# Kernel optimization log

Measured on AMD Instinct MI355X. Metric: run time of the kernel, lower is better.

## Reference

```python
import jax, jax.numpy as jnp
import numpy as np
import math

D, H, DK, DFF, B, T, K = 512, 8, 64, 2048, 8, 512, 31
P = 2 * T - 1  # rel-pos length


def _ln(x, g, b, eps=1e-5):
    mu = jnp.mean(x, -1, keepdims=True)
    var = jnp.var(x, -1, keepdims=True)
    return (x - mu) * jax.lax.rsqrt(var + eps) * g + b


def _silu(x):
    return x * jax.nn.sigmoid(x)


def _rel_shift(x):
    # x: [B,H,T,P] -> NeMo-style relative shift
    b, h, t, p = x.shape
    x = jnp.pad(x, ((0, 0), (0, 0), (0, 0), (1, 0)))
    x = x.reshape(b, h, p + 1, t)
    return x[:, :, 1:, :].reshape(b, h, t, p)


def _forward(x, pos_emb, ln1_g, ln1_b, ff1_w1, ff1_b1, ff1_w2, ff1_b2,
             lna_g, lna_b, wq, bq, wk, bk, wv, bv, wo, bo, wpos, pbu, pbv,
             lnc_g, lnc_b, pw1_w, pw1_b, dw_w, dw_b, cln_g, cln_b, pw2_w, pw2_b,
             ln2_g, ln2_b, ff2_w1, ff2_b1, ff2_w2, ff2_b2, lno_g, lno_b):
    b, t, d = x.shape
    h, dk = pbu.shape
    # FF1 (half-step residual)
    r = x
    y = _ln(x, ln1_g, ln1_b)
    y = _silu(y @ ff1_w1 + ff1_b1) @ ff1_w2 + ff1_b2
    r = r + 0.5 * y
    # Rel-pos multi-head attention
    y = _ln(r, lna_g, lna_b)
    q = (y @ wq + bq).reshape(b, t, h, dk)
    k = (y @ wk + bk).reshape(b, t, h, dk)
    v = (y @ wv + bv).reshape(b, t, h, dk)
    p = (pos_emb @ wpos).reshape(pos_emb.shape[0], -1, h, dk)[0]  # [P,H,dk]
    ac = jnp.einsum('bthd,bshd->bhts', q + pbu, k)
    bd = jnp.einsum('bthd,phd->bhtp', q + pbv, p)
    bd = _rel_shift(bd)[..., :t]
    attn = jax.nn.softmax((ac + bd) / math.sqrt(dk), axis=-1)
    o = jnp.einsum('bhts,bshd->bthd', attn, v).reshape(b, t, d) @ wo + bo
    r = r + o
    # Conformer convolution module (layer_norm variant)
    y = _ln(r, lnc_g, lnc_b)
    y = y @ pw1_w + pw1_b                       # [B,T,2D] pointwise conv1
    a, g = jnp.split(y, 2, axis=-1)
    y = a * jax.nn.sigmoid(g)                   # GLU over channels
    y = jnp.transpose(y, (0, 2, 1))             # [B,D,T]
    pad = (dw_w.shape[1] - 1) // 2
    y = jax.lax.conv_general_dilated(
        y, dw_w[:, None, :], (1,), [(pad, pad)],
        feature_group_count=d, dimension_numbers=('NCH', 'OIH', 'NCH'))
    y = y + dw_b[None, :, None]
    y = jnp.transpose(y, (0, 2, 1))             # [B,T,D]
    y = _ln(y, cln_g, cln_b)
    y = _silu(y) @ pw2_w + pw2_b                # pointwise conv2
    r = r + y
    # FF2 (half-step residual)
    y = _ln(r, ln2_g, ln2_b)
    y = _silu(y @ ff2_w1 + ff2_b1) @ ff2_w2 + ff2_b2
    r = r + 0.5 * y
    return _ln(r, lno_g, lno_b)


def setup_inputs() -> dict:
    key = jax.random.key(0)
    ks = iter(jax.random.split(key, 64))
    rn = lambda shape, s=0.05: jax.random.normal(next(ks), shape, dtype=jnp.float32) * s
    ones = lambda n: jnp.ones((n,), jnp.float32)
    zeros = lambda n: jnp.zeros((n,), jnp.float32)
    return dict(
        x=jax.random.normal(next(ks), (B, T, D), jnp.float32),
        pos_emb=jax.random.normal(next(ks), (1, P, D), jnp.float32),
        ln1_g=ones(D), ln1_b=zeros(D),
        ff1_w1=rn((D, DFF)), ff1_b1=zeros(DFF), ff1_w2=rn((DFF, D)), ff1_b2=zeros(D),
        lna_g=ones(D), lna_b=zeros(D),
        wq=rn((D, D)), bq=zeros(D), wk=rn((D, D)), bk=zeros(D),
        wv=rn((D, D)), bv=zeros(D), wo=rn((D, D)), bo=zeros(D),
        wpos=rn((D, D)), pbu=rn((H, DK)), pbv=rn((H, DK)),
        lnc_g=ones(D), lnc_b=zeros(D),
        pw1_w=rn((D, 2 * D)), pw1_b=zeros(2 * D),
        dw_w=rn((D, K)), dw_b=zeros(D),
        cln_g=ones(D), cln_b=zeros(D),
        pw2_w=rn((D, D)), pw2_b=zeros(D),
        ln2_g=ones(D), ln2_b=zeros(D),
        ff2_w1=rn((D, DFF)), ff2_b1=zeros(DFF), ff2_w2=rn((DFF, D)), ff2_b2=zeros(D),
        lno_g=ones(D), lno_b=zeros(D))


def reference(x, pos_emb, ln1_g, ln1_b, ff1_w1, ff1_b1, ff1_w2, ff1_b2,
              lna_g, lna_b, wq, bq, wk, bk, wv, bv, wo, bo, wpos, pbu, pbv,
              lnc_g, lnc_b, pw1_w, pw1_b, dw_w, dw_b, cln_g, cln_b, pw2_w, pw2_b,
              ln2_g, ln2_b, ff2_w1, ff2_b1, ff2_w2, ff2_b2, lno_g, lno_b):
    return _forward(x, pos_emb, ln1_g, ln1_b, ff1_w1, ff1_b1, ff1_w2, ff1_b2,
                    lna_g, lna_b, wq, bq, wk, bk, wv, bv, wo, bo, wpos, pbu, pbv,
                    lnc_g, lnc_b, pw1_w, pw1_b, dw_w, dw_b, cln_g, cln_b, pw2_w, pw2_b,
                    ln2_g, ln2_b, ff2_w1, ff2_b1, ff2_w2, ff2_b2, lno_g, lno_b)
```

## Files before the change

kernel.cpp:

```cpp
#include <hip/hip_runtime.h>
#include <hip/hip_bf16.h>

#define Bb 8
#define Tt 512
#define Dd 512
#define Hh 8
#define DKk 64
#define DFFf 2048
#define Pp 1023
#define KCc 31
#define BTt 4096
#define QS 1536

typedef __hip_bfloat16 bf16;
typedef __attribute__((ext_vector_type(8))) short short8;
typedef __attribute__((ext_vector_type(4))) short s4v;
typedef __attribute__((ext_vector_type(4))) float f32x4;

union BFU { __hip_bfloat16 h; short s; };
static __device__ __forceinline__ short bfbits(float f) {
    BFU u; u.h = __float2bfloat16(f); return u.s;
}
static __device__ __forceinline__ float bff(short s) {
    BFU u; u.s = s; return __bfloat162float(u.h);
}
static __device__ __forceinline__ unsigned pk2(float a, float b) {
    return (unsigned)(unsigned short)bfbits(a) | ((unsigned)(unsigned short)bfbits(b) << 16);
}

static __device__ __forceinline__ int dflag(const void* lg) {
    return ((const unsigned*)lg)[0] == 0x3F803F80u;
}

#define GLD16(g, l) __builtin_amdgcn_global_load_lds(                          \
    (const __attribute__((address_space(1))) void*)(g),                        \
    (__attribute__((address_space(3))) void*)(l), 16, 0, 0)

struct CvtDesc { const void* src; unsigned n; unsigned off; unsigned startBlk; };
struct CvtArgs { CvtDesc d[32]; };

__global__ __launch_bounds__(256) void cvt_batch_k(CvtArgs args, int ncv,
                                                   bf16* __restrict__ dst,
                                                   const void* __restrict__ lg) {
    int bid = blockIdx.x;
    int ti = 0;
    while (ti + 1 < ncv && bid >= (int)args.d[ti + 1].startBlk) ti++;
    CvtDesc de = args.d[ti];
    unsigned i = (bid - de.startBlk) * 256u + threadIdx.x;
    if (i >= de.n) return;
    float v;
    if (dflag(lg)) v = __bfloat162float(((const bf16*)de.src)[i]);
    else           v = ((const float*)de.src)[i];
    dst[de.off + i] = __float2bfloat16(v);
}

struct TD { const void* src; unsigned doff, R, C, startBlk; };
struct TArgs { TD d[11]; };

__global__ __launch_bounds__(256) void transpose_batch_k(TArgs ta, bf16* __restrict__ wt,
                                                         const void* __restrict__ lg) {
    int bid = blockIdx.x;
    int ti = 0;
    while (ti + 1 < 11 && bid >= (int)ta.d[ti + 1].startBlk) ti++;
    TD t = ta.d[ti];
    int tile = bid - t.startBlk;
    int ntc = t.C >> 5;
    int tr = tile / ntc, tc = tile % ntc;
    __shared__ short tl[32][33];
    short* out = (short*)wt + t.doff;
    int tx = threadIdx.x & 31, ty = threadIdx.x >> 5;
    int fl = dflag(lg);
#pragma unroll
    for (int i = 0; i < 32; i += 8) {
        size_t idx = (size_t)(tr * 32 + ty + i) * t.C + tc * 32 + tx;
        short v;
        if (fl) v = ((const short*)t.src)[idx];
        else    v = bfbits(((const float*)t.src)[idx]);
        tl[ty + i][tx] = v;
    }
    __syncthreads();
#pragma unroll
    for (int i = 0; i < 32; i += 8)
        out[(size_t)(tc * 32 + ty + i) * t.R + tr * 32 + tx] = tl[tx][ty + i];
}

__global__ __launch_bounds__(256) void prep_misc_k(const void* __restrict__ dww, bf16* __restrict__ dwT,
                                                   const void* __restrict__ bq, const void* __restrict__ bk,
                                                   const void* __restrict__ bv, bf16* __restrict__ bqkv,
                                                   const void* __restrict__ lg) {
    int i = blockIdx.x * 256 + threadIdx.x;
    int fl = dflag(lg);
    if (i < Dd * KCc) {
        int d = i / KCc, j = i % KCc;
        short v = fl ? ((const short*)dww)[i] : bfbits(((const float*)dww)[i]);
        ((short*)dwT)[j * Dd + d] = v;
    } else {
        int j = i - Dd * KCc;
        if (j < QS) {
            const void* s = (j < 512) ? bq : ((j < 1024) ? bk : bv);
            int idx = j & 511;
            short v = fl ? ((const short*)s)[idx] : bfbits(((const float*)s)[idx]);
            ((short*)bqkv)[j] = v;
        }
    }
}

template <int SILU>
__global__ __launch_bounds__(256) void ln_k(const float* __restrict__ in,
                                            const bf16* __restrict__ g,
                                            const bf16* __restrict__ b,
                                            bf16* __restrict__ out) {
    int row = blockIdx.x;
    int tid = threadIdx.x;
    float2 v = ((const float2*)(in + (size_t)row * Dd))[tid];
    float s = v.x + v.y;
    float ss = v.x * v.x + v.y * v.y;
#pragma unroll
    for (int off = 32; off > 0; off >>= 1) {
        s += __shfl_xor(s, off);
        ss += __shfl_xor(ss, off);
    }
    __shared__ float red[2][4];
    int wid = tid >> 6;
    if ((tid & 63) == 0) { red[0][wid] = s; red[1][wid] = ss; }
    __syncthreads();
    float S = red[0][0] + red[0][1] + red[0][2] + red[0][3];
    float SS = red[1][0] + red[1][1] + red[1][2] + red[1][3];
    float mean = S * (1.0f / Dd);
    float var = SS * (1.0f / Dd) - mean * mean;
    float rstd = rsqrtf(var + 1e-5f);
    unsigned gp = *(const unsigned*)((const short*)g + 2 * tid);
    unsigned bp = *(const unsigned*)((const short*)b + 2 * tid);
    float o0 = (v.x - mean) * rstd * bff((short)(gp & 0xFFFF)) + bff((short)(bp & 0xFFFF));
    float o1 = (v.y - mean) * rstd * bff((short)(gp >> 16)) + bff((short)(bp >> 16));
    if (SILU) {
        o0 = o0 / (1.0f + __expf(-o0));
        o1 = o1 / (1.0f + __expf(-o1));
    }
    *(unsigned*)((short*)out + (size_t)row * Dd + 2 * tid) = pk2(o0, o1);
}

__global__ __launch_bounds__(256) void ln_x_k(const void* __restrict__ x,
                                              const bf16* __restrict__ g,
                                              const bf16* __restrict__ b,
                                              float* __restrict__ r,
                                              bf16* __restrict__ out,
                                              const void* __restrict__ lg) {
    int row = blockIdx.x;
    int tid = threadIdx.x;
    size_t base = (size_t)row * Dd;
    float v0, v1;
    if (dflag(lg)) {
        unsigned xp = *(const unsigned*)((const short*)x + base + 2 * tid);
        v0 = bff((short)(xp & 0xFFFF));
        v1 = bff((short)(xp >> 16));
    } else {
        float2 xv = ((const float2*)((const float*)x + base))[tid];
        v0 = xv.x; v1 = xv.y;
    }
    ((float2*)(r + base))[tid] = make_float2(v0, v1);
    float s = v0 + v1;
    float ss = v0 * v0 + v1 * v1;
#pragma unroll
    for (int off = 32; off > 0; off >>= 1) {
        s += __shfl_xor(s, off);
        ss += __shfl_xor(ss, off);
    }
    __shared__ float red[2][4];
    int wid = tid >> 6;
    if ((tid & 63) == 0) { red[0][wid] = s; red[1][wid] = ss; }
    __syncthreads();
    float S = red[0][0] + red[0][1] + red[0][2] + red[0][3];
    float SS = red[1][0] + red[1][1] + red[1][2] + red[1][3];
    float mean = S * (1.0f / Dd);
    float var = SS * (1.0f / Dd) - mean * mean;
    float rstd = rsqrtf(var + 1e-5f);
    unsigned gp = *(const unsigned*)((const short*)g + 2 * tid);
    unsigned bp = *(const unsigned*)((const short*)b + 2 * tid);
    float o0 = (v0 - mean) * rstd * bff((short)(gp & 0xFFFF)) + bff((short)(bp & 0xFFFF));
    float o1 = (v1 - mean) * rstd * bff((short)(gp >> 16)) + bff((short)(bp >> 16));
    *(unsigned*)((short*)out + base + 2 * tid) = pk2(o0, o1);
}

__global__ __launch_bounds__(256) void ln_out_k(const float* __restrict__ in,
                                                const bf16* __restrict__ g,
                                                const bf16* __restrict__ b,
                                                void* __restrict__ out,
                                                const void* __restrict__ lg) {
    int row = blockIdx.x;
    int tid = threadIdx.x;
    size_t base = (size_t)row * Dd;
    float2 v = ((const float2*)(in + base))[tid];
    float s = v.x + v.y;
    float ss = v.x * v.x + v.y * v.y;
#pragma unroll
    for (int off = 32; off > 0; off >>= 1) {
        s += __shfl_xor(s, off);
        ss += __shfl_xor(ss, off);
    }
    __shared__ float red[2][4];
    int wid = tid >> 6;
    if ((tid & 63) == 0) { red[0][wid] = s; red[1][wid] = ss; }
    __syncthreads();
    float S = red[0][0] + red[0][1] + red[0][2] + red[0][3];
    float SS = red[1][0] + red[1][1] + red[1][2] + red[1][3];
    float mean = S * (1.0f / Dd);
    float var = SS * (1.0f / Dd) - mean * mean;
    float rstd = rsqrtf(var + 1e-5f);
    unsigned gp = *(const unsigned*)((const short*)g + 2 * tid);
    unsigned bp = *(const unsigned*)((const short*)b + 2 * tid);
    float o0 = (v.x - mean) * rstd * bff((short)(gp & 0xFFFF)) + bff((short)(bp & 0xFFFF));
    float o1 = (v.y - mean) * rstd * bff((short)(gp >> 16)) + bff((short)(bp >> 16));
    if (dflag(lg)) {
        *(unsigned*)((short*)out + base + 2 * tid) = pk2(o0, o1);
    } else {
        ((float2*)((float*)out + base))[tid] = make_float2(o0, o1);
    }
}

template <int BM, int BN, int BK, int WM, int WN, typename CT, int ACT, int RES, int VT>
__global__ __launch_bounds__(256) void gemm_mfma_k(const bf16* __restrict__ Abf,
                                                   const bf16* __restrict__ WT,
                                                   const bf16* __restrict__ bias,
                                                   const float* __restrict__ resid,
                                                   CT* __restrict__ C,
                                                   bf16* __restrict__ vt,
                                                   int M, int N, int Kd, float alpha) {
    constexpr int MT = WM / 16, NT = WN / 16;
    constexpr int WX = BN / WN;
    constexpr int CPB = BK / 8;
    constexpr int KS = BK / 32;
    __shared__ __align__(16) short As[BM * BK];
    __shared__ __align__(16) short Bs[BN * BK];
    int tid = threadIdx.x;
    int wid = tid >> 6, lane = tid & 63;
    int lm = lane & 15, quad = lane >> 4;
    int wy = wid / WX, wx = wid % WX;
    int bm = blockIdx.y * BM, bn = blockIdx.x * BN;
    const short* Ag = (const short*)Abf;
    const short* Bg = (const short*)WT;

    f32x4 acc[MT][NT] = {};

    for (int k0 = 0; k0 < Kd; k0 += BK) {
#pragma unroll
        for (int it = 0; it < BM * CPB / 256; it++) {
            int c = it * 256 + tid;
            int row = c / CPB;
            int q = (c % CPB) ^ (row & 7);
            int gr = bm + row;
            if (gr > M - 1) gr = M - 1;
            GLD16(Ag + (size_t)gr * Kd + k0 + q * 8, As + (it * 256 + wid * 64) * 8);
        }
#pragma unroll
        for (int it = 0; it < BN * CPB / 256; it++) {
            int c = it * 256 + tid;
            int row = c / CPB;
            int q = (c % CPB) ^ (row & 7);
            GLD16(Bg + (size_t)(bn + row) * Kd + k0 + q * 8, Bs + (it * 256 + wid * 64) * 8);
        }
        __syncthreads();
        short8 af[MT][KS], bfv[NT][KS];
#pragma unroll
        for (int mt = 0; mt < MT; mt++) {
            int row = wy * WM + mt * 16 + lm;
#pragma unroll
            for (int ks = 0; ks < KS; ks++)
                af[mt][ks] = *(const short8*)&As[row * BK + (((ks * 4 + quad) ^ (row & 7)) * 8)];
        }
#pragma unroll
        for (int nt = 0; nt < NT; nt++) {
            int row = wx * WN + nt * 16 + lm;
#pragma unroll
            for (int ks = 0; ks < KS; ks++)
                bfv[nt][ks] = *(const short8*)&Bs[row * BK + (((ks * 4 + quad) ^ (row & 7)) * 8)];
        }
#pragma unroll
        for (int ks = 0; ks < KS; ks++)
#pragma unroll
            for (int mt = 0; mt < MT; mt++)
#pragma unroll
                for (int nt = 0; nt < NT; nt++)
                    acc[mt][nt] = __builtin_amdgcn_mfma_f32_16x16x32_bf16(af[mt][ks], bfv[nt][ks], acc[mt][nt], 0, 0, 0);
        __syncthreads();
    }

#pragma unroll
    for (int mt = 0; mt < MT; mt++) {
#pragma unroll
        for (int nt = 0; nt < NT; nt++) {
            int gcol = bn + wx * WN + nt * 16 + lm;
            int growb = bm + wy * WM + mt * 16 + quad * 4;
            if (VT && gcol >= 1024) {
                float bi = bias ? __bfloat162float(bias[gcol]) : 0.f;
                s4v pk;
#pragma unroll
                for (int r = 0; r < 4; r++) pk[r] = bfbits(acc[mt][nt][r] + bi);
                *(s4v*)((short*)vt + (size_t)((growb >> 9) * 512 + (gcol - 1024)) * 512 + (growb & 511)) = pk;
            } else {
#pragma unroll
                for (int r = 0; r < 4; r++) {
                    int grow = growb + r;
                    if (grow >= M) continue;
                    float v = acc[mt][nt][r];
                    if (bias) v += __bfloat162float(bias[gcol]);
                    if (ACT == 1) v = v / (1.0f + __expf(-v));
                    if (RES == 1) v = resid[(size_t)grow * N + gcol] + alpha * v;
                    C[(size_t)grow * N + gcol] = (CT)v;
                }
            }
        }
    }
}

__global__ __launch_bounds__(256) void gemm_glu_k(const bf16* __restrict__ Abf,
                                                  const bf16* __restrict__ WT,
                                                  const bf16* __restrict__ bias,
                                                  bf16* __restrict__ C) {
    constexpr int BM = 64, BN = 64, BK = 64, WM = 32, WN = 32;
    constexpr int MT = WM / 16, NT = WN / 16, WX = BN / WN, CPB = BK / 8, KS = BK / 32;
    __shared__ __align__(16) short As[BM * BK];
    __shared__ __align__(16) short Bs[2 * BN * BK];
    int tid = threadIdx.x;
    int wid = tid >> 6, lane = tid & 63;
    int lm = lane & 15, quad = lane >> 4;
    int wy = wid / WX, wx = wid % WX;
    int bm = blockIdx.y * BM, bn = blockIdx.x * BN;
    const short* Ag = (const short*)Abf;
    const short* Bg = (const short*)WT;

    f32x4 acc[MT][NT][2] = {};

    for (int k0 = 0; k0 < Dd; k0 += BK) {
#pragma unroll
        for (int it = 0; it < BM * CPB / 256; it++) {
            int c = it * 256 + tid;
            int row = c / CPB;
            int q = (c % CPB) ^ (row & 7);
            GLD16(Ag + (size_t)(bm + row) * Dd + k0 + q * 8, As + (it * 256 + wid * 64) * 8);
        }
#pragma unroll
        for (int it = 0; it < 2 * BN * CPB / 256; it++) {
            int c = it * 256 + tid;
            int row = c / CPB;
            int q = (c % CPB) ^ (row & 7);
            int wrow = (row < BN) ? (bn + row) : (512 + bn + row - BN);
            GLD16(Bg + (size_t)wrow * Dd + k0 + q * 8, Bs + (it * 256 + wid * 64) * 8);
        }
        __syncthreads();
        short8 af[MT][KS], bfv[NT][2][KS];
#pragma unroll
        for (int mt = 0; mt < MT; mt++) {
            int row = wy * WM + mt * 16 + lm;
#pragma unroll
            for (int ks = 0; ks < KS; ks++)
                af[mt][ks] = *(const short8*)&As[row * BK + (((ks * 4 + quad) ^ (row & 7)) * 8)];
        }
#pragma unroll
        for (int nt = 0; nt < NT; nt++) {
#pragma unroll
            for (int hf = 0; hf < 2; hf++) {
                int row = hf * BN + wx * WN + nt * 16 + lm;
#pragma unroll
                for (int ks = 0; ks < KS; ks++)
                    bfv[nt][hf][ks] = *(const short8*)&Bs[row * BK + (((ks * 4 + quad) ^ (row & 7)) * 8)];
            }
        }
#pragma unroll
        for (int ks = 0; ks < KS; ks++)
#pragma unroll
            for (int mt = 0; mt < MT; mt++)
#pragma unroll
                for (int nt = 0; nt < NT; nt++) {
                    acc[mt][nt][0] = __builtin_amdgcn_mfma_f32_16x16x32_bf16(af[mt][ks], bfv[nt][0][ks], acc[mt][nt][0], 0, 0, 0);
                    acc[mt][nt][1] = __builtin_amdgcn_mfma_f32_16x16x32_bf16(af[mt][ks], bfv[nt][1][ks], acc[mt][nt][1], 0, 0, 0);
                }
        __syncthreads();
    }

#pragma unroll
    for (int mt = 0; mt < MT; mt++) {
#pragma unroll
        for (int nt = 0; nt < NT; nt++) {
#pragma unroll
            for (int r = 0; r < 4; r++) {
                int grow = bm + wy * WM + mt * 16 + quad * 4 + r;
                int gcol = bn + wx * WN + nt * 16 + lm;
                float va = acc[mt][nt][0][r] + __bfloat162float(bias[gcol]);
                float vg = acc[mt][nt][1][r] + __bfloat162float(bias[512 + gcol]);
                float v = va / (1.0f + __expf(-vg));
                C[(size_t)grow * Dd + gcol] = __float2bfloat16(v);
            }
        }
    }
}

#define SST 516

__global__ __launch_bounds__(256, 4) void attn_mfma_k(const bf16* __restrict__ qkv,
                                                      const bf16* __restrict__ p,
                                                      const bf16* __restrict__ vT,
                                                      const bf16* __restrict__ pbu,
                                                      const bf16* __restrict__ pbv,
                                                      bf16* __restrict__ out) {
    __shared__ float S[16][SST];
    __shared__ float lsum[16];
    short* Pbase = (short*)&S[0][0];
    int tid = threadIdx.x;
    int wid = tid >> 6;
    int lane = tid & 63;
    int lm = lane & 15;
    int quad = lane >> 4;
    int bidx = blockIdx.x;
    int b = bidx >> 8;
    int h = (bidx >> 5) & 7;
    int t0 = (bidx & 31) * 16;

    const short* qkvs = (const short*)qkv;
    const short* ps = (const short*)p;

    short8 qu[2], qv[2];
    {
        size_t rowbase = ((size_t)(b * Tt + t0 + lm) * QS) + h * DKk;
        const short* pbus = (const short*)pbu + h * DKk + quad * 8;
        const short* pbvs = (const short*)pbv + h * DKk + quad * 8;
#pragma unroll
        for (int ksp = 0; ksp < 2; ksp++) {
            short8 raw = *(const short8*)(qkvs + rowbase + ksp * 32 + quad * 8);
            short8 bu = *(const short8*)(pbus + ksp * 32);
            short8 bv = *(const short8*)(pbvs + ksp * 32);
#pragma unroll
            for (int j = 0; j < 8; j++) {
                float qf = bff(raw[j]);
                qu[ksp][j] = bfbits(qf + bff(bu[j]));
                qv[ksp][j] = bfbits(qf + bff(bv[j]));
            }
        }
    }

    const float scale = 0.125f;

    int pb0 = 511 - t0 + wid * 128;

    f32x4 dprev = {0.f, 0.f, 0.f, 0.f};
    {
        int prow = pb0 - 16 + lm;
        if (prow < 0) prow = 0;
        size_t pa = (size_t)prow * Dd + h * DKk;
#pragma unroll
        for (int ksp = 0; ksp < 2; ksp++) {
            short8 pf = *(const short8*)(ps + pa + ksp * 32 + quad * 8);
            dprev = __builtin_amdgcn_mfma_f32_16x16x32_bf16(qv[ksp], pf, dprev, 0, 0, 0);
        }
    }

#pragma unroll
    for (int i = 0; i < 8; i++) {
        int st = wid * 8 + i;
        f32x4 ac = {0.f, 0.f, 0.f, 0.f};
        f32x4 dcur = {0.f, 0.f, 0.f, 0.f};
        size_t krow = ((size_t)(b * Tt + st * 16 + lm) * QS) + 512 + h * DKk;
        size_t pa = (size_t)(pb0 + i * 16 + lm) * Dd + h * DKk;
#pragma unroll
        for (int ksp = 0; ksp < 2; ksp++) {
            short8 kf = *(const short8*)(qkvs + krow + ksp * 32 + quad * 8);
            short8 pf = *(const short8*)(ps + pa + ksp * 32 + quad * 8);
            ac = __builtin_amdgcn_mfma_f32_16x16x32_bf16(qu[ksp], kf, ac, 0, 0, 0);
            dcur = __builtin_amdgcn_mfma_f32_16x16x32_bf16(qv[ksp], pf, dcur, 0, 0, 0);
        }
#pragma unroll
        for (int r = 0; r < 4; r++) {
            int m = quad * 4 + r;
            int j = (lm - m) & 15;
            int srcl = quad * 16 + j;
            float b2 = __shfl(dcur[r], srcl, 64);
            float b1 = __shfl(dprev[r], srcl, 64);
            float bd = (lm >= m) ? b2 : b1;
            S[m][st * 16 + lm] = scale * (ac[r] + bd);
        }
        dprev = dcur;
    }
    __syncthreads();

    {
        int srow = tid >> 4;
        int g2 = (tid & 15) * 2;
        float vals[32];
        float mx = -1e30f;
#pragma unroll
        for (int i = 0; i < 16; i++) {
            float2 v = *(const float2*)&S[srow][i * 32 + g2];
            vals[2 * i] = v.x;
            vals[2 * i + 1] = v.y;
            mx = fmaxf(mx, fmaxf(v.x, v.y));
        }
#pragma unroll
        for (int off = 1; off < 16; off <<= 1) mx = fmaxf(mx, __shfl_xor(mx, off));
        float sum = 0.f;
        short* prow = Pbase + (size_t)srow * (SST * 2);
#pragma unroll
        for (int i = 0; i < 16; i++) {
            float e0 = __expf(vals[2 * i] - mx);
            float e1 = __expf(vals[2 * i + 1] - mx);
            sum += e0 + e1;
            *(unsigned*)&prow[i * 32 + g2] = pk2(e0, e1);
        }
#pragma unroll
        for (int off = 1; off < 16; off <<= 1) sum += __shfl_xor(sum, off);
        if (g2 == 0) lsum[srow] = sum;
    }
    __syncthreads();

    int d0 = wid * 16;
    f32x4 o = {0.f, 0.f, 0.f, 0.f};
    const short* vrow = (const short*)vT + ((size_t)(b * Hh + h) * DKk + d0 + lm) * Tt;
    const short* parow = Pbase + (size_t)lm * (SST * 2);
#pragma unroll
    for (int ksp = 0; ksp < 16; ksp++) {
        int kk = ksp * 32 + quad * 8;
        short8 a = *(const short8*)(parow + kk);
        short8 bf = *(const short8*)(vrow + kk);
        o = __builtin_amdgcn_mfma_f32_16x16x32_bf16(a, bf, o, 0, 0, 0);
    }
    short* os = (short*)out;
#pragma unroll
    for (int r = 0; r < 4; r++) {
        int m = quad * 4 + r;
        os[((size_t)(b * Tt + t0 + m) * Dd) + h * DKk + d0 + lm] = bfbits(o[r] / lsum[m]);
    }
}

__global__ __launch_bounds__(256) void dwconv_ln_k(const bf16* __restrict__ in,
                                                   const bf16* __restrict__ wT,
                                                   const bf16* __restrict__ bdw,
                                                   const bf16* __restrict__ g,
                                                   const bf16* __restrict__ bb,
                                                   bf16* __restrict__ out) {
    int row = blockIdx.x * 4 + (threadIdx.x >> 6);
    int lane = threadIdx.x & 63;
    int d0 = lane * 8;
    int t = row & 511, b = row >> 9;
    const short* ins = (const short*)in + (size_t)b * Tt * Dd;
    const short* wts = (const short*)wT;
    float acc[8];
    short8 bv = *(const short8*)((const short*)bdw + d0);
#pragma unroll
    for (int e = 0; e < 8; e++) acc[e] = bff(bv[e]);
#pragma unroll
    for (int j = 0; j < KCc; j++) {
        int tt = t + j - 15;
        if (tt < 0 || tt >= Tt) continue;
        short8 iv = *(const short8*)(ins + (size_t)tt * Dd + d0);
        short8 wv = *(const short8*)(wts + j * Dd + d0);
#pragma unroll
        for (int e = 0; e < 8; e++) acc[e] += bff(iv[e]) * bff(wv[e]);
    }
    float s = 0.f, ss = 0.f;
#pragma unroll
    for (int e = 0; e < 8; e++) { s += acc[e]; ss += acc[e] * acc[e]; }
#pragma unroll
    for (int off = 32; off > 0; off >>= 1) {
        s += __shfl_xor(s, off);
        ss += __shfl_xor(ss, off);
    }
    float mean = s * (1.0f / Dd);
    float var = ss * (1.0f / Dd) - mean * mean;
    float rstd = rsqrtf(var + 1e-5f);
    short8 gv = *(const short8*)((const short*)g + d0);
    short8 bbv = *(const short8*)((const short*)bb + d0);
    short8 ov;
#pragma unroll
    for (int e = 0; e < 8; e++) {
        float o = (acc[e] - mean) * rstd * bff(gv[e]) + bff(bbv[e]);
        o = o / (1.0f + __expf(-o));
        ov[e] = bfbits(o);
    }
    *(short8*)((short*)out + (size_t)row * Dd + d0) = ov;
}

extern "C" void kernel_launch(void* const* d_in, const int* in_sizes, int n_in,
                              void* d_out, int out_size, void* d_ws, size_t ws_size,
                              hipStream_t stream) {
    char* base = (char*)d_ws;
    bf16* wb = (bf16*)(base + 256);

    size_t woff[39];
    size_t acc = 0;
    for (int i = 1; i < 39; i++) { woff[i] = acc; acc += (size_t)in_sizes[i]; }
    size_t wbytes = (2 * acc + 255) & ~(size_t)255;

    const size_t NBT = (size_t)BTt * Dd;
    float* r   = (float*)((char*)wb + wbytes);
    bf16* a    = (bf16*)((char*)r + NBT * 4);
    bf16* big  = a + NBT;
    bf16* pbuf = big + (size_t)BTt * DFFf;
    bf16* wt   = pbuf + (size_t)Pp * Dd;

    const void* lg = d_in[2];

    bf16* c_pos   = wb + woff[1];
    bf16* c_ln1g  = wb + woff[2],  *c_ln1b = wb + woff[3];
    bf16* c_f1b1  = wb + woff[5];
    bf16* c_f1b2  = wb + woff[7];
    bf16* c_lnag  = wb + woff[8],  *c_lnab = wb + woff[9];
    bf16* c_bo    = wb + woff[17];
    bf16* c_pbu   = wb + woff[19], *c_pbv  = wb + woff[20];
    bf16* c_lncg  = wb + woff[21], *c_lncb = wb + woff[22];
    bf16* c_p1b   = wb + woff[24];
    bf16* c_dwb   = wb + woff[26];
    bf16* c_clng  = wb + woff[27], *c_clnb = wb + woff[28];
    bf16* c_p2b   = wb + woff[30];
    bf16* c_ln2g  = wb + woff[31], *c_ln2b = wb + woff[32];
    bf16* c_f2b1  = wb + woff[34];
    bf16* c_f2b2  = wb + woff[36];
    bf16* c_lnog  = wb + woff[37], *c_lnob = wb + woff[38];

    const int tin[11]  = {4, 6, 10, 12, 14, 16, 18, 23, 29, 33, 35};
    const unsigned tR[11] = {512, 2048, 512, 512, 512, 512, 512, 512, 512, 512, 2048};
    const unsigned tC[11] = {2048, 512, 512, 512, 512, 512, 512, 1024, 512, 2048, 512};
    size_t toff[11]; size_t tacc = 0;
    for (int i = 0; i < 11; i++) { toff[i] = tacc; tacc += (size_t)tR[i] * tC[i]; }
    bf16* t_f1w1 = wt + toff[0];
    bf16* t_f1w2 = wt + toff[1];
    bf16* t_wqkv = wt + toff[2];
    bf16* t_wo   = wt + toff[5];
    bf16* t_wpos = wt + toff[6];
    bf16* t_p1w  = wt + toff[7];
    bf16* t_p2w  = wt + toff[8];
    bf16* t_f2w1 = wt + toff[9];
    bf16* t_f2w2 = wt + toff[10];
    bf16* bias_qkv = wt + tacc;
    bf16* dwT      = bias_qkv + QS;
    bf16* vTb      = dwT + KCc * Dd;

    dim3 blk(256);

    bool skip[39] = {};
    for (int i = 0; i < 11; i++) skip[tin[i]] = true;
    skip[11] = skip[13] = skip[15] = skip[25] = true;
    CvtArgs ca;
    int ncv = 0;
    unsigned blkacc = 0;
    for (int i = 1; i < 39; i++) {
        if (skip[i]) continue;
        ca.d[ncv].src = d_in[i];
        ca.d[ncv].n = (unsigned)in_sizes[i];
        ca.d[ncv].off = (unsigned)woff[i];
        ca.d[ncv].startBlk = blkacc;
        blkacc += (unsigned)((in_sizes[i] + 255) / 256);
        ncv++;
    }
    cvt_batch_k<<<blkacc, blk, 0, stream>>>(ca, ncv, wb, lg);

    TArgs ta;
    unsigned tblk = 0;
    for (int i = 0; i < 11; i++) {
        ta.d[i].src = d_in[tin[i]];
        ta.d[i].doff = (unsigned)toff[i];
        ta.d[i].R = tR[i];
        ta.d[i].C = tC[i];
        ta.d[i].startBlk = tblk;
        tblk += (tR[i] >> 5) * (tC[i] >> 5);
    }
    transpose_batch_k<<<tblk, blk, 0, stream>>>(ta, wt, lg);
    prep_misc_k<<<(Dd * KCc + QS + 255) / 256, blk, 0, stream>>>(
        d_in[25], dwT, d_in[11], d_in[13], d_in[15], bias_qkv, lg);

    auto g128 = [](int M, int N) { return dim3(N / 128, M / 128); };
    auto g64  = [](int M, int N) { return dim3(N / 64, (M + 63) / 64); };

    ln_x_k<<<BTt, blk, 0, stream>>>(d_in[0], c_ln1g, c_ln1b, r, a, lg);
    gemm_mfma_k<128, 128, 64, 64, 64, bf16, 1, 0, 0><<<g128(BTt, DFFf), blk, 0, stream>>>(
        a, t_f1w1, c_f1b1, nullptr, big, nullptr, BTt, DFFf, Dd, 0.f);
    gemm_mfma_k<64, 64, 128, 32, 32, float, 0, 1, 0><<<g64(BTt, Dd), blk, 0, stream>>>(
        big, t_f1w2, c_f1b2, r, r, nullptr, BTt, Dd, DFFf, 0.5f);

    bf16* qkvb = big;
    bf16* cb   = big + 3 * NBT;
    ln_k<0><<<BTt, blk, 0, stream>>>(r, c_lnag, c_lnab, a);
    gemm_mfma_k<128, 64, 64, 64, 32, bf16, 0, 0, 1><<<dim3(QS / 64, BTt / 128), blk, 0, stream>>>(
        a, t_wqkv, bias_qkv, nullptr, qkvb, vTb, BTt, QS, Dd, 0.f);
    gemm_mfma_k<64, 64, 64, 32, 32, bf16, 0, 0, 0><<<g64(Pp, Dd), blk, 0, stream>>>(
        c_pos, t_wpos, nullptr, nullptr, pbuf, nullptr, Pp, Dd, Dd, 0.f);
    attn_mfma_k<<<Bb * Hh * (Tt / 16), blk, 0, stream>>>(qkvb, pbuf, vTb, c_pbu, c_pbv, cb);
    gemm_mfma_k<64, 64, 64, 32, 32, float, 0, 1, 0><<<g64(BTt, Dd), blk, 0, stream>>>(
        cb, t_wo, c_bo, r, r, nullptr, BTt, Dd, Dd, 1.0f);

    bf16* gluo = big + 2 * NBT;
    ln_k<0><<<BTt, blk, 0, stream>>>(r, c_lncg, c_lncb, a);
    gemm_glu_k<<<dim3(Dd / 64, BTt / 64), blk, 0, stream>>>(a, t_p1w, c_p1b, gluo);
    dwconv_ln_k<<<BTt / 4, blk, 0, stream>>>(gluo, dwT, c_dwb, c_clng, c_clnb, a);
    gemm_mfma_k<64, 64, 64, 32, 32, float, 0, 1, 0><<<g64(BTt, Dd), blk, 0, stream>>>(
        a, t_p2w, c_p2b, r, r, nullptr, BTt, Dd, Dd, 1.0f);

    ln_k<0><<<BTt, blk, 0, stream>>>(r, c_ln2g, c_ln2b, a);
    gemm_mfma_k<128, 128, 64, 64, 64, bf16, 1, 0, 0><<<g128(BTt, DFFf), blk, 0, stream>>>(
        a, t_f2w1, c_f2b1, nullptr, big, nullptr, BTt, DFFf, Dd, 0.f);
    gemm_mfma_k<64, 64, 128, 32, 32, float, 0, 1, 0><<<g64(BTt, Dd), blk, 0, stream>>>(
        big, t_f2w2, c_f2b2, r, r, nullptr, BTt, Dd, DFFf, 0.5f);

    ln_out_k<<<BTt, blk, 0, stream>>>(r, c_lnog, c_lnob, d_out, lg);
}
```

Measured before the change: 439.4 us.

## Keep attention scores in registers and shrink LDS to a bf16 probability tile

The attention kernel keeps the 16x512 score tile in per-wave registers instead of writing fp32 scores to shared memory. Row max and sum are computed with cross-lane shuffles plus a small cross-wave reduction through LDS, and only bf16 exponentials are stored. This cuts LDS use from about 33KB to about 17KB, which allows raising the launch bound from 4 to 6 blocks per CU. It also remaps block indices so that consecutive blocks span batches, and splits the PV MFMA chain into two accumulators to give more instruction-level parallelism. The cost is higher register pressure from holding 32 floats of scores per lane.

```diff
diff --git a/kernel.cpp b/kernel.cpp
--- a/kernel.cpp
+++ b/kernel.cpp
@@ -395,23 +395,23 @@
     }
 }
 
-#define SST 516
-
-__global__ __launch_bounds__(256, 4) void attn_mfma_k(const bf16* __restrict__ qkv,
+#define PST 520
+
+__global__ __launch_bounds__(256, 6) void attn_mfma_k(const bf16* __restrict__ qkv,
                                                       const bf16* __restrict__ p,
                                                       const bf16* __restrict__ vT,
                                                       const bf16* __restrict__ pbu,
                                                       const bf16* __restrict__ pbv,
                                                       bf16* __restrict__ out) {
-    __shared__ float S[16][SST];
-    __shared__ float lsum[16];
-    short* Pbase = (short*)&S[0][0];
+    __shared__ __align__(16) short Pl[16 * PST];
+    __shared__ __align__(16) float redm[16][4];
+    __shared__ __align__(16) float reds[16][4];
     int tid = threadIdx.x;
     int wid = tid >> 6;
     int lane = tid & 63;
     int lm = lane & 15;
     int quad = lane >> 4;
-    int bidx = blockIdx.x;
+    int bidx = (blockIdx.x & 7) * 256 + (blockIdx.x >> 3);
     int b = bidx >> 8;
     int h = (bidx >> 5) & 7;
     int t0 = (bidx & 31) * 16;
@@ -439,35 +439,29 @@
     }
 
     const float scale = 0.125f;
-
     int pb0 = 511 - t0 + wid * 128;
 
     f32x4 dprev = {0.f, 0.f, 0.f, 0.f};
     {
         int prow = pb0 - 16 + lm;
         if (prow < 0) prow = 0;
-        size_t pa = (size_t)prow * Dd + h * DKk;
-#pragma unroll
-        for (int ksp = 0; ksp < 2; ksp++) {
-            short8 pf = *(const short8*)(ps + pa + ksp * 32 + quad * 8);
-            dprev = __builtin_amdgcn_mfma_f32_16x16x32_bf16(qv[ksp], pf, dprev, 0, 0, 0);
-        }
-    }
-
+        const short* pa = ps + (size_t)prow * Dd + h * DKk + quad * 8;
+        dprev = __builtin_amdgcn_mfma_f32_16x16x32_bf16(qv[0], *(const short8*)pa, dprev, 0, 0, 0);
+        dprev = __builtin_amdgcn_mfma_f32_16x16x32_bf16(qv[1], *(const short8*)(pa + 32), dprev, 0, 0, 0);
+    }
+
+    f32x4 sreg[8];
 #pragma unroll
     for (int i = 0; i < 8; i++) {
         int st = wid * 8 + i;
         f32x4 ac = {0.f, 0.f, 0.f, 0.f};
         f32x4 dcur = {0.f, 0.f, 0.f, 0.f};
-        size_t krow = ((size_t)(b * Tt + st * 16 + lm) * QS) + 512 + h * DKk;
-        size_t pa = (size_t)(pb0 + i * 16 + lm) * Dd + h * DKk;
-#pragma unroll
-        for (int ksp = 0; ksp < 2; ksp++) {
-            short8 kf = *(const short8*)(qkvs + krow + ksp * 32 + quad * 8);
-            short8 pf = *(const short8*)(ps + pa + ksp * 32 + quad * 8);
-            ac = __builtin_amdgcn_mfma_f32_16x16x32_bf16(qu[ksp], kf, ac, 0, 0, 0);
-            dcur = __builtin_amdgcn_mfma_f32_16x16x32_bf16(qv[ksp], pf, dcur, 0, 0, 0);
-        }
+        const short* ka = qkvs + ((size_t)(b * Tt + st * 16 + lm) * QS) + 512 + h * DKk + quad * 8;
+        const short* pa = ps + (size_t)(pb0 + i * 16 + lm) * Dd + h * DKk + quad * 8;
+        ac = __builtin_amdgcn_mfma_f32_16x16x32_bf16(qu[0], *(const short8*)ka, ac, 0, 0, 0);
+        ac = __builtin_amdgcn_mfma_f32_16x16x32_bf16(qu[1], *(const short8*)(ka + 32), ac, 0, 0, 0);
+        dcur = __builtin_amdgcn_mfma_f32_16x16x32_bf16(qv[0], *(const short8*)pa, dcur, 0, 0, 0);
+        dcur = __builtin_amdgcn_mfma_f32_16x16x32_bf16(qv[1], *(const short8*)(pa + 32), dcur, 0, 0, 0);
 #pragma unroll
         for (int r = 0; r < 4; r++) {
             int m = quad * 4 + r;
@@ -476,57 +470,82 @@
             float b2 = __shfl(dcur[r], srcl, 64);
             float b1 = __shfl(dprev[r], srcl, 64);
             float bd = (lm >= m) ? b2 : b1;
-            S[m][st * 16 + lm] = scale * (ac[r] + bd);
+            sreg[i][r] = scale * (ac[r] + bd);
         }
         dprev = dcur;
     }
+
+    float mrow[4];
+#pragma unroll
+    for (int r = 0; r < 4; r++) {
+        float m = sreg[0][r];
+#pragma unroll
+        for (int i = 1; i < 8; i++) m = fmaxf(m, sreg[i][r]);
+#pragma unroll
+        for (int off = 1; off < 16; off <<= 1) m = fmaxf(m, __shfl_xor(m, off));
+        mrow[r] = m;
+    }
+    if (lm < 4) {
+        float v = (lm == 0) ? mrow[0] : (lm == 1) ? mrow[1] : (lm == 2) ? mrow[2] : mrow[3];
+        redm[quad * 4 + lm][wid] = v;
+    }
     __syncthreads();
 
-    {
-        int srow = tid >> 4;
-        int g2 = (tid & 15) * 2;
-        float vals[32];
-        float mx = -1e30f;
-#pragma unroll
-        for (int i = 0; i < 16; i++) {
-            float2 v = *(const float2*)&S[srow][i * 32 + g2];
-            vals[2 * i] = v.x;
-            vals[2 * i + 1] = v.y;
-            mx = fmaxf(mx, fmaxf(v.x, v.y));
-        }
-#pragma unroll
-        for (int off = 1; off < 16; off <<= 1) mx = fmaxf(mx, __shfl_xor(mx, off));
-        float sum = 0.f;
-        short* prow = Pbase + (size_t)srow * (SST * 2);
-#pragma unroll
-        for (int i = 0; i < 16; i++) {
-            float e0 = __expf(vals[2 * i] - mx);
-            float e1 = __expf(vals[2 * i + 1] - mx);
-            sum += e0 + e1;
-            *(unsigned*)&prow[i * 32 + g2] = pk2(e0, e1);
-        }
-#pragma unroll
-        for (int off = 1; off < 16; off <<= 1) sum += __shfl_xor(sum, off);
-        if (g2 == 0) lsum[srow] = sum;
+    float gm[4], srow[4];
+#pragma unroll
+    for (int r = 0; r < 4; r++) {
+        float4 mv = *(const float4*)&redm[quad * 4 + r][0];
+        gm[r] = fmaxf(fmaxf(mv.x, mv.y), fmaxf(mv.z, mv.w));
+        srow[r] = 0.f;
+    }
+#pragma unroll
+    for (int i = 0; i < 8; i++) {
+        int col = (wid * 8 + i) * 16 + lm;
+#pragma unroll
+        for (int r = 0; r < 4; r++) {
+            float e = __expf(sreg[i][r] - gm[r]);
+            srow[r] += e;
+            Pl[(quad * 4 + r) * PST + col] = bfbits(e);
+        }
+    }
+#pragma unroll
+    for (int r = 0; r < 4; r++) {
+#pragma unroll
+        for (int off = 1; off < 16; off <<= 1) srow[r] += __shfl_xor(srow[r], off);
+    }
+    if (lm < 4) {
+        float v = (lm == 0) ? srow[0] : (lm == 1) ? srow[1] : (lm == 2) ? srow[2] : srow[3];
+        reds[quad * 4 + lm][wid] = v;
     }
     __syncthreads();
 
+    float lsum[4];
+#pragma unroll
+    for (int r = 0; r < 4; r++) {
+        float4 sv = *(const float4*)&reds[quad * 4 + r][0];
+        lsum[r] = (sv.x + sv.y) + (sv.z + sv.w);
+    }
+
     int d0 = wid * 16;
-    f32x4 o = {0.f, 0.f, 0.f, 0.f};
     const short* vrow = (const short*)vT + ((size_t)(b * Hh + h) * DKk + d0 + lm) * Tt;
-    const short* parow = Pbase + (size_t)lm * (SST * 2);
-#pragma unroll
-    for (int ksp = 0; ksp < 16; ksp++) {
-        int kk = ksp * 32 + quad * 8;
-        short8 a = *(const short8*)(parow + kk);
-        short8 bf = *(const short8*)(vrow + kk);
-        o = __builtin_amdgcn_mfma_f32_16x16x32_bf16(a, bf, o, 0, 0, 0);
-    }
+    const short* parow = Pl + (size_t)lm * PST;
+    f32x4 o0 = {0.f, 0.f, 0.f, 0.f};
+    f32x4 o1 = {0.f, 0.f, 0.f, 0.f};
+#pragma unroll
+    for (int ksp = 0; ksp < 16; ksp += 2) {
+        short8 a0 = *(const short8*)(parow + ksp * 32 + quad * 8);
+        short8 v0 = *(const short8*)(vrow + ksp * 32 + quad * 8);
+        short8 a1 = *(const short8*)(parow + (ksp + 1) * 32 + quad * 8);
+        short8 v1 = *(const short8*)(vrow + (ksp + 1) * 32 + quad * 8);
+        o0 = __builtin_amdgcn_mfma_f32_16x16x32_bf16(a0, v0, o0, 0, 0, 0);
+        o1 = __builtin_amdgcn_mfma_f32_16x16x32_bf16(a1, v1, o1, 0, 0, 0);
+    }
+    f32x4 o = o0 + o1;
     short* os = (short*)out;
 #pragma unroll
     for (int r = 0; r < 4; r++) {
         int m = quad * 4 + r;
-        os[((size_t)(b * Tt + t0 + m) * Dd) + h * DKk + d0 + lm] = bfbits(o[r] / lsum[m]);
+        os[((size_t)(b * Tt + t0 + m) * Dd) + h * DKk + d0 + lm] = bfbits(o[r] / lsum[r]);
     }
 }
 
```

Result: no change. 432.2 us (-1.6%).
